# Kernel tuning notes

Measured on AMD Instinct MI355X. Metric: run time of the kernel, lower is better.

The kernel has to match this reference:

```python
import jax, jax.numpy as jnp
import numpy as np

B, S, D, H, G = 4, 2048, 1024, 16, 32
HD = D // H
LN_EPS = 1e-5


def _lin_init(key, fan_in, fan_out):
    kw, kb = jax.random.split(key)
    bound = 1.0 / np.sqrt(fan_in)
    W = jax.random.uniform(kw, (fan_in, fan_out), jnp.float32, -bound, bound)
    b = jax.random.uniform(kb, (fan_out,), jnp.float32, -bound, bound)
    return W, b


def setup_inputs() -> dict:
    key = jax.random.key(0)
    ks = jax.random.split(key, 9)
    x = jax.random.normal(ks[0], (B, S, D), jnp.float32)
    geo_features = jax.random.normal(ks[1], (B, G), jnp.float32)
    Wq, bq = _lin_init(ks[2], D, D)
    Wk, bk = _lin_init(ks[3], D, D)
    Wv, bv = _lin_init(ks[4], D, D)
    Wo, bo = _lin_init(ks[5], D, D)
    ge_W1, ge_b1 = _lin_init(ks[6], G, D)
    ln_g = jnp.ones((D,), jnp.float32)
    ln_b = jnp.zeros((D,), jnp.float32)
    ge_W2, ge_b2 = _lin_init(ks[7], D, D)
    gm_W, gm_b = _lin_init(ks[8], D, H)
    return dict(x=x, geo_features=geo_features, Wq=Wq, bq=bq, Wk=Wk, bk=bk,
                Wv=Wv, bv=bv, Wo=Wo, bo=bo, ge_W1=ge_W1, ge_b1=ge_b1,
                ln_g=ln_g, ln_b=ln_b, ge_W2=ge_W2, ge_b2=ge_b2,
                gm_W=gm_W, gm_b=gm_b)


def reference(x, geo_features, Wq, bq, Wk, bk, Wv, bv, Wo, bo,
              ge_W1, ge_b1, ln_g, ln_b, ge_W2, ge_b2, gm_W, gm_b):
    # QKV projections -> (B, H, S, HD)
    def split_heads(t):
        return t.reshape(B, S, H, HD).transpose(0, 2, 1, 3)
    Q = split_heads(x @ Wq + bq)
    K = split_heads(x @ Wk + bk)
    V = split_heads(x @ Wv + bv)

    # geo encoder: Linear -> LayerNorm -> ReLU -> Linear
    h = geo_features @ ge_W1 + ge_b1                      # (B, D)
    mu = jnp.mean(h, axis=-1, keepdims=True)
    var = jnp.mean(jnp.square(h - mu), axis=-1, keepdims=True)
    h = (h - mu) / jnp.sqrt(var + LN_EPS) * ln_g + ln_b
    h = jax.nn.relu(h)
    geo_encoded = h @ ge_W2 + ge_b2                       # (B, D)
    geo_mod = jax.nn.sigmoid(geo_encoded @ gm_W + gm_b)   # (B, H)

    scale = 1.0 / np.sqrt(HD)
    scores = jnp.einsum('bhqd,bhkd->bhqk', Q, K) * scale  # (B, H, S, S)
    scores = scores * (1.0 + geo_mod[:, :, None, None])
    attn = jax.nn.softmax(scores, axis=-1)                # dropout in eval mode: identity
    ctx = jnp.einsum('bhqk,bhkd->bhqd', attn, V)          # (B, H, S, HD)
    ctx = ctx.transpose(0, 2, 1, 3).reshape(B, S, D)
    out = ctx @ Wo + bo
    return out, attn
```

## Files before the change

kernel.cpp:

```cpp
#include <hip/hip_runtime.h>

typedef __attribute__((ext_vector_type(8))) short bf16x8;
typedef __attribute__((ext_vector_type(4))) float f32x4;
typedef __attribute__((ext_vector_type(4))) unsigned short us4;
typedef unsigned short u16;

#define MB (1024*1024)

#define WAITV(N) asm volatile("s_waitcnt vmcnt(" #N ")" ::: "memory")
#define WAITL0() asm volatile("s_waitcnt lgkmcnt(0)" ::: "memory")
#define BAR()    __builtin_amdgcn_s_barrier()
#define SCHEDB() __builtin_amdgcn_sched_barrier(0)

__device__ __forceinline__ u16 f2bf(float f) {
    unsigned u = __float_as_uint(f);
    unsigned r = (u + 0x7fffu + ((u >> 16) & 1u)) >> 16;
    return (u16)r;
}

__device__ __forceinline__ unsigned cvtpk(float a, float b) {
    unsigned r;
    asm("v_cvt_pk_bf16_f32 %0, %1, %2" : "=v"(r) : "v"(a), "v"(b));
    return r;
}

__device__ __forceinline__ f32x4 mfma16(bf16x8 a, bf16x8 b, f32x4 c) {
    return __builtin_amdgcn_mfma_f32_16x16x32_bf16(a, b, c, 0, 0, 0);
}

__device__ __forceinline__ void gload16(const void* g, void* l) {
    __builtin_amdgcn_global_load_lds(
        (__attribute__((address_space(1))) void*)(unsigned long long)g,
        (__attribute__((address_space(3))) void*)l, 16, 0, 0);
}

__global__ __launch_bounds__(256) void k_cvtx(const float* __restrict__ x, u16* __restrict__ xb) {
    const long long i = (long long)blockIdx.x * 256 + threadIdx.x;
    const float4* xp = (const float4*)x;
    float4 a = xp[i*2], b = xp[i*2+1];
    bf16x8 o;
    o[0]=(short)f2bf(a.x); o[1]=(short)f2bf(a.y); o[2]=(short)f2bf(a.z); o[3]=(short)f2bf(a.w);
    o[4]=(short)f2bf(b.x); o[5]=(short)f2bf(b.y); o[6]=(short)f2bf(b.z); o[7]=(short)f2bf(b.w);
    *(bf16x8*)&xb[i*8] = o;
}

__global__ __launch_bounds__(256) void k_wtcvt(const float* __restrict__ W0, const float* __restrict__ W1,
                                               const float* __restrict__ W2, const float* __restrict__ W3,
                                               u16* __restrict__ wt) {
    __shared__ float tl[32][33];
    const int t = threadIdx.x, z = blockIdx.z;
    const float* W = (z==0)?W0:(z==1)?W1:(z==2)?W2:W3;
    const int k0 = blockIdx.x*32, n0 = blockIdx.y*32;
    const int r = t >> 3, c4 = (t & 7) * 4;
    float4 v = *(const float4*)&W[(long long)(k0+r)*1024 + n0 + c4];
    tl[r][c4] = v.x; tl[r][c4+1] = v.y; tl[r][c4+2] = v.z; tl[r][c4+3] = v.w;
    __syncthreads();
    us4 ov;
    ov[0] = f2bf(tl[c4+0][r]); ov[1] = f2bf(tl[c4+1][r]);
    ov[2] = f2bf(tl[c4+2][r]); ov[3] = f2bf(tl[c4+3][r]);
    *(us4*)&wt[((long long)z << 20) + (long long)(n0+r)*1024 + k0 + c4] = ov;
}

__global__ __launch_bounds__(1024) void k_geo1(const float* __restrict__ geo, const float* __restrict__ W1,
                                               const float* __restrict__ b1, const float* __restrict__ lng,
                                               const float* __restrict__ lnb, float* __restrict__ hr) {
    const int b = blockIdx.x, j = threadIdx.x;
    float acc = b1[j];
    #pragma unroll 8
    for (int g = 0; g < 32; ++g) acc += geo[b*32+g] * W1[(long long)g*1024 + j];
    float s1 = acc, s2 = acc*acc;
    #pragma unroll
    for (int m = 1; m < 64; m <<= 1) { s1 += __shfl_xor(s1, m); s2 += __shfl_xor(s2, m); }
    __shared__ float r1[16], r2[16];
    __shared__ float mu_s, rv_s;
    const int wid = j >> 6, lid = j & 63;
    if (lid == 0) { r1[wid] = s1; r2[wid] = s2; }
    __syncthreads();
    if (j == 0) {
        float S1 = 0.f, S2 = 0.f;
        for (int i = 0; i < 16; ++i) { S1 += r1[i]; S2 += r2[i]; }
        float mu = S1 / 1024.f;
        float var = S2 / 1024.f - mu*mu;
        mu_s = mu; rv_s = rsqrtf(var + 1e-5f);
    }
    __syncthreads();
    float hv = (acc - mu_s) * rv_s * lng[j] + lnb[j];
    hr[b*1024 + j] = fmaxf(hv, 0.f);
}

__global__ __launch_bounds__(256) void k_geo2(const float* __restrict__ hr, const float* __restrict__ W2,
                                              const float* __restrict__ b2, float* __restrict__ ge) {
    const int b = blockIdx.x >> 4, jc = blockIdx.x & 15;
    const int t = threadIdx.x;
    __shared__ float hs[1024];
    __shared__ float parts[4][64];
    #pragma unroll
    for (int i = 0; i < 4; ++i) hs[t*4 + i] = hr[b*1024 + t*4 + i];
    __syncthreads();
    const int j = jc*64 + (t & 63), dq = t >> 6;
    float acc = 0.f;
    #pragma unroll 16
    for (int dd = 0; dd < 256; ++dd) {
        const int d = dq*256 + dd;
        acc += hs[d] * W2[(long long)d*1024 + j];
    }
    parts[dq][t & 63] = acc;
    __syncthreads();
    if (t < 64) {
        const int jj = jc*64 + t;
        ge[b*1024 + jj] = b2[jj] + parts[0][t] + parts[1][t] + parts[2][t] + parts[3][t];
    }
}

__global__ __launch_bounds__(1024) void k_geo3(const float* __restrict__ ge, const float* __restrict__ gmW,
                                               const float* __restrict__ gmb, float* __restrict__ qs) {
    const int t = threadIdx.x;
    const int hh = t & 15, b = (t >> 4) & 3, dq = t >> 6;
    __shared__ float parts[16][64];
    float part = 0.f;
    #pragma unroll 16
    for (int dd = 0; dd < 64; ++dd) {
        const int d = dq*64 + dd;
        part += ge[b*1024 + d] * gmW[d*16 + hh];
    }
    parts[dq][b*16 + hh] = part;
    __syncthreads();
    if (t < 64) {
        float s = gmb[t & 15];
        #pragma unroll
        for (int k = 0; k < 16; ++k) s += parts[k][t];
        qs[t] = 0.125f * (1.f + 1.f/(1.f + __expf(-s)));
    }
}

__global__ __launch_bounds__(256) void k_qkv_gemm(const u16* __restrict__ xb, const u16* __restrict__ wtq,
                                                  const float* __restrict__ bq, const float* __restrict__ bk,
                                                  const float* __restrict__ bv, u16* __restrict__ outq) {
    __shared__ u16 lA[128*64];
    __shared__ u16 lB[128*64];
    const int t = threadIdx.x, z = blockIdx.z;
    const int m0 = blockIdx.y * 128, n0 = blockIdx.x * 128;
    const u16* wt = wtq + (long long)z * (1024*1024);
    const float* bias = (z==0) ? bq : (z==1) ? bk : bv;
    u16* out = outq + (long long)z * 8388608;
    const int w = t >> 6, l = t & 63, lm = l & 15, lg = l >> 4;
    const int wr = (w >> 1) * 64, wc = (w & 1) * 64;
    f32x4 acc[4][4] = {};
    const char* gA = (const char*)xb + (long long)(m0 + (t>>3))*2048 + (t&7)*16;
    const char* gB = (const char*)wt + (long long)(n0 + (t>>3))*2048 + (t&7)*16;
    char* lAp = (char*)lA + t*16;
    char* lBp = (char*)lB + t*16;
    for (int k0 = 0; k0 < 1024; k0 += 64) {
        #pragma unroll
        for (int i = 0; i < 4; ++i) {
            gload16(gA + (long long)i*32*2048, lAp + i*4096);
            gload16(gB + (long long)i*32*2048, lBp + i*4096);
        }
        gA += 128; gB += 128;
        __syncthreads();
        #pragma unroll
        for (int kk = 0; kk < 2; ++kk) {
            bf16x8 af[4], bfr[4];
            #pragma unroll
            for (int mi = 0; mi < 4; ++mi)
                af[mi] = *(const bf16x8*)((const char*)lA + (wr + mi*16 + lm)*128 + kk*64 + lg*16);
            #pragma unroll
            for (int ni = 0; ni < 4; ++ni)
                bfr[ni] = *(const bf16x8*)((const char*)lB + (wc + ni*16 + lm)*128 + kk*64 + lg*16);
            #pragma unroll
            for (int mi = 0; mi < 4; ++mi)
                #pragma unroll
                for (int ni = 0; ni < 4; ++ni)
                    acc[mi][ni] = mfma16(bfr[ni], af[mi], acc[mi][ni]);
        }
        __syncthreads();
    }
    #pragma unroll
    for (int mi = 0; mi < 4; ++mi) {
        const int m = m0 + wr + mi*16 + lm;
        const int b = m >> 11, s = m & 2047;
        #pragma unroll
        for (int ni = 0; ni < 4; ++ni) {
            const int nb = n0 + wc + ni*16 + lg*4;
            const float4 bn4 = *(const float4*)&bias[nb];
            const int hh = nb >> 6, d = nb & 63;
            uint2 pk;
            pk.x = cvtpk(acc[mi][ni][0] + bn4.x, acc[mi][ni][1] + bn4.y);
            pk.y = cvtpk(acc[mi][ni][2] + bn4.z, acc[mi][ni][3] + bn4.w);
            *(uint2*)&out[(((long long)b*16 + hh)*2048 + s)*64 + d] = pk;
        }
    }
}

__global__ __launch_bounds__(256) void k_vtrans(const u16* __restrict__ vb, u16* __restrict__ vt) {
    __shared__ u16 tl[64][40];
    const int t = threadIdx.x;
    const int bh = blockIdx.z, s0 = blockIdx.y*64, d0 = blockIdx.x*32;
    const u16* vsrc = vb + (long long)bh*2048*64;
    {
        const int sl = t >> 2, dg = t & 3;
        bf16x8 v = *(const bf16x8*)&vsrc[(long long)(s0+sl)*64 + d0 + dg*8];
        *(bf16x8*)&tl[sl][dg*8] = v;
    }
    __syncthreads();
    {
        const int dl = t >> 3, sg = t & 7;
        bf16x8 o;
        #pragma unroll
        for (int j = 0; j < 8; ++j) o[j] = (short)tl[sg*8+j][dl];
        *(bf16x8*)&vt[((long long)bh*64 + d0+dl)*2048 + s0 + sg*8] = o;
    }
}

__global__ __launch_bounds__(512, 4) void k_attn_ctx(const u16* __restrict__ Qb, const u16* __restrict__ Kb,
                                                     const u16* __restrict__ Vt, const float* __restrict__ qsv,
                                                     float* __restrict__ invg, u16* __restrict__ ctxb) {
    __shared__ char lds[81920];

    const int nl = blockIdx.x;
    const int ob = (nl & 7)*64 + (nl >> 3);
    const int bh = ob >> 3, qt = ob & 7;
    const int t = threadIdx.x, w = t >> 6, l = t & 63, lm = l & 15, lg = l >> 4;
    const int q0 = qt * 256;
    const float qs = qsv[bh];

    const char* KB = (const char*)Kb + (long long)bh * 262144;
    const char* VB = (const char*)Vt + (long long)bh * 262144;

    bf16x8 qf[2][2];
    {
        const char* QB = (const char*)Qb + (long long)bh * 262144;
        #pragma unroll
        for (int ms = 0; ms < 2; ++ms)
            #pragma unroll
            for (int kc = 0; kc < 2; ++kc)
                qf[ms][kc] = *(const bf16x8*)(QB + (long long)(q0 + w*32 + ms*16 + lm)*128 + kc*64 + lg*16);
    }

    const int off = t*16;
    const int row = off >> 7, cbyt = off & 127;
    const int offA = off;
    const int srcK = row*128  + (cbyt ^ ((row & 7) << 4));
    const int srcV = row*4096 + (cbyt ^ ((row & 7) << 4));

    char* lP = lds + 49152;
    float lsum[2] = {0.f, 0.f};
    f32x4 cacc[2][4] = {};

    gload16(KB + srcK, lds + offA);
    gload16(VB + srcV, lds + 24576 + offA);
    gload16(KB + 8192 + srcK, lds + 8192 + offA);
    gload16(VB + 128 + srcV, lds + 24576 + 8192 + offA);
    SCHEDB();
    WAITV(2); BAR(); SCHEDB();

    int cb_ = 0, sb_ = 2;
    for (int kt = 0; kt < 32; ++kt) {
        const int ktn = (kt < 30) ? kt + 2 : 31;
        gload16(KB + (long long)ktn*8192 + srcK, lds + sb_*8192 + offA);
        gload16(VB + (long long)ktn*128 + srcV, lds + 24576 + sb_*8192 + offA);
        SCHEDB();

        const char* kb = lds + cb_*8192;
        #pragma unroll
        for (int ns = 0; ns < 4; ++ns) {
            const int rowb = ns*16 + lm;
            const int tag = (rowb & 7) << 4;
            bf16x8 kf0 = *(const bf16x8*)(kb + rowb*128 + ((lg*16) ^ tag));
            bf16x8 kf1 = *(const bf16x8*)(kb + rowb*128 + ((64 + lg*16) ^ tag));
            #pragma unroll
            for (int ms = 0; ms < 2; ++ms) {
                f32x4 a = {};
                a = mfma16(kf0, qf[ms][0], a);
                a = mfma16(kf1, qf[ms][1], a);
                const float p0 = __expf(a[0]*qs);
                const float p1 = __expf(a[1]*qs);
                const float p2 = __expf(a[2]*qs);
                const float p3 = __expf(a[3]*qs);
                lsum[ms] += (p0 + p1) + (p2 + p3);
                const int prow = w*32 + ms*16 + lm;
                const int ptag = (prow & 7) << 4;
                uint2 pk; pk.x = cvtpk(p0, p1); pk.y = cvtpk(p2, p3);
                *(uint2*)(lP + prow*128 + ((32*ns + 8*lg) ^ ptag)) = pk;
            }
        }
        WAITL0(); SCHEDB();

        const char* vb = lds + 24576 + cb_*8192;
        #pragma unroll
        for (int ks = 0; ks < 2; ++ks) {
            bf16x8 pa[2];
            #pragma unroll
            for (int ms = 0; ms < 2; ++ms) {
                const int prow = w*32 + ms*16 + lm;
                pa[ms] = *(const bf16x8*)(lP + prow*128 + ((ks*64 + lg*16) ^ ((prow & 7) << 4)));
            }
            #pragma unroll
            for (int dn = 0; dn < 4; ++dn) {
                const int rv = dn*16 + lm;
                bf16x8 vf = *(const bf16x8*)(vb + rv*128 + ((ks*64 + lg*16) ^ ((rv & 7) << 4)));
                cacc[0][dn] = mfma16(pa[0], vf, cacc[0][dn]);
                cacc[1][dn] = mfma16(pa[1], vf, cacc[1][dn]);
            }
        }
        WAITV(2); BAR(); SCHEDB();
        cb_ = (cb_ == 2) ? 0 : cb_ + 1;
        sb_ = (sb_ == 2) ? 0 : sb_ + 1;
    }

    float invl[2];
    #pragma unroll
    for (int ms = 0; ms < 2; ++ms) {
        float v = lsum[ms];
        v += __shfl_xor(v, 16);
        v += __shfl_xor(v, 32);
        invl[ms] = 1.f / v;
    }
    if (lg == 0) {
        invg[bh*2048 + q0 + w*32 + lm]      = invl[0];
        invg[bh*2048 + q0 + w*32 + 16 + lm] = invl[1];
    }
    float* fs = (float*)(lP + w*4096);
    if (lg == 0) { fs[lm] = invl[0]; fs[16 + lm] = invl[1]; }
    WAITL0(); SCHEDB();
    f32x4 iv[2];
    iv[0] = *(const f32x4*)&fs[lg*4];
    iv[1] = *(const f32x4*)&fs[16 + lg*4];

    const int b = bh >> 4, hh = bh & 15;
    #pragma unroll
    for (int ms = 0; ms < 2; ++ms)
        #pragma unroll
        for (int dn = 0; dn < 4; ++dn)
            #pragma unroll
            for (int r = 0; r < 4; ++r) {
                const int q = q0 + w*32 + ms*16 + lg*4 + r;
                ctxb[(((long long)b*2048 + q)*16 + hh)*64 + dn*16 + lm] = f2bf(cacc[ms][dn][r] * iv[ms][r]);
            }
}

__global__ __launch_bounds__(256, 2) void k_pwrite(const u16* __restrict__ Qb, const u16* __restrict__ Kb,
                                                   const float* __restrict__ qsv, const float* __restrict__ invg,
                                                   float* __restrict__ attn_out) {
    __shared__ char lds[81920];

    const int nl = blockIdx.x;
    const int ob = (nl & 7)*512 + (nl >> 3);
    const int bh = ob >> 6, qt = ob & 63;
    const int t = threadIdx.x, w = t >> 6, l = t & 63, lm = l & 15, lg = l >> 4;
    const int q0 = qt * 32;
    const int qg = w & 1, kq = w >> 1;
    const float qs = qsv[bh];

    const char* KB = (const char*)Kb + (long long)bh * 262144;

    bf16x8 qf[2];
    {
        const char* QB = (const char*)Qb + (long long)bh * 262144;
        #pragma unroll
        for (int kc = 0; kc < 2; ++kc)
            qf[kc] = *(const bf16x8*)(QB + (long long)(q0 + qg*16 + lm)*128 + kc*64 + lg*16);
    }
    const float invq = invg[bh*2048 + q0 + qg*16 + lm];

    int offA[2], srcK[2];
    #pragma unroll
    for (int i = 0; i < 2; ++i) {
        const int off = i*4096 + t*16;
        const int row = off >> 7, cbyt = off & 127;
        offA[i] = off;
        srcK[i] = row*128 + (cbyt ^ ((row & 7) << 4));
    }

    char* lP = lds + 49152;

    #pragma unroll
    for (int tt = 0; tt < 5; ++tt)
        #pragma unroll
        for (int i = 0; i < 2; ++i)
            gload16(KB + (long long)tt*8192 + srcK[i], lds + tt*8192 + offA[i]);
    SCHEDB();

    for (int kt = 0; kt < 32; ++kt) {
        if (kt < 4)            { WAITV(8); }
        else if ((kt & 3) == 0){ WAITV(24); }
        else                   { WAITV(16); }
        BAR(); SCHEDB();

        {
            const int ktn = (kt + 5 < 32) ? kt + 5 : 31;
            char* dst = lds + ((kt + 5) % 6)*8192;
            #pragma unroll
            for (int i = 0; i < 2; ++i)
                gload16(KB + (long long)ktn*8192 + srcK[i], dst + offA[i]);
        }
        SCHEDB();

        const char* kb = lds + (kt % 6)*8192;
        #pragma unroll
        for (int ns = 0; ns < 2; ++ns) {
            const int rowb = kq*32 + ns*16 + lm;
            const int tag = (lm & 7) << 4;
            bf16x8 kf0 = *(const bf16x8*)(kb + rowb*128 + ((lg*16) ^ tag));
            bf16x8 kf1 = *(const bf16x8*)(kb + rowb*128 + ((64 + lg*16) ^ tag));
            f32x4 a = {};
            a = mfma16(kf0, qf[0], a);
            a = mfma16(kf1, qf[1], a);
            f32x4 pv4;
            pv4[0] = __expf(a[0]*qs) * invq;
            pv4[1] = __expf(a[1]*qs) * invq;
            pv4[2] = __expf(a[2]*qs) * invq;
            pv4[3] = __expf(a[3]*qs) * invq;
            const int prow = qg*16 + lm;
            const int kwb = ((kt & 3) << 8) + (kq << 7) + (ns << 6) + (lg << 4);
            *(f32x4*)(lP + prow*1024 + (kwb ^ (lm << 4))) = pv4;
        }

        if ((kt & 3) == 3) {
            const int win = kt >> 2;
            WAITL0(); BAR(); SCHEDB();
            const int r0 = w*8;
            #pragma unroll
            for (int r = 0; r < 8; ++r) {
                const int rr = r0 + r;
                f32x4 v = *(const f32x4*)(lP + rr*1024 + ((l*16) ^ ((rr & 15) << 4)));
                *(f32x4*)(attn_out + ((long long)(bh*2048 + q0 + rr))*2048 + win*256 + l*4) = v;
            }
            SCHEDB();
        }
    }
}

__global__ __launch_bounds__(256) void k_o_gemm(const u16* __restrict__ ab, const u16* __restrict__ wt,
                                                const float* __restrict__ bo, float* __restrict__ outf) {
    __shared__ u16 lA[128*64];
    __shared__ u16 lB[128*64];
    const int t = threadIdx.x;
    const int m0 = blockIdx.y * 128, n0 = blockIdx.x * 128;
    const int w = t >> 6, l = t & 63, lm = l & 15, lg = l >> 4;
    const int wr = (w >> 1) * 64, wc = (w & 1) * 64;
    f32x4 acc[4][4] = {};
    const char* gA = (const char*)ab + (long long)(m0 + (t>>3))*2048 + (t&7)*16;
    const char* gB = (const char*)wt + (long long)(n0 + (t>>3))*2048 + (t&7)*16;
    char* lAp = (char*)lA + t*16;
    char* lBp = (char*)lB + t*16;
    for (int k0 = 0; k0 < 1024; k0 += 64) {
        #pragma unroll
        for (int i = 0; i < 4; ++i) {
            gload16(gA + (long long)i*32*2048, lAp + i*4096);
            gload16(gB + (long long)i*32*2048, lBp + i*4096);
        }
        gA += 128; gB += 128;
        __syncthreads();
        #pragma unroll
        for (int kk = 0; kk < 2; ++kk) {
            bf16x8 af[4], bfr[4];
            #pragma unroll
            for (int mi = 0; mi < 4; ++mi)
                af[mi] = *(const bf16x8*)((const char*)lA + (wr + mi*16 + lm)*128 + kk*64 + lg*16);
            #pragma unroll
            for (int ni = 0; ni < 4; ++ni)
                bfr[ni] = *(const bf16x8*)((const char*)lB + (wc + ni*16 + lm)*128 + kk*64 + lg*16);
            #pragma unroll
            for (int mi = 0; mi < 4; ++mi)
                #pragma unroll
                for (int ni = 0; ni < 4; ++ni)
                    acc[mi][ni] = mfma16(bfr[ni], af[mi], acc[mi][ni]);
        }
        __syncthreads();
    }
    #pragma unroll
    for (int mi = 0; mi < 4; ++mi) {
        const int m = m0 + wr + mi*16 + lm;
        #pragma unroll
        for (int ni = 0; ni < 4; ++ni) {
            const int nb = n0 + wc + ni*16 + lg*4;
            const float4 bn4 = *(const float4*)&bo[nb];
            f32x4 v = acc[mi][ni];
            v[0] += bn4.x; v[1] += bn4.y; v[2] += bn4.z; v[3] += bn4.w;
            *(f32x4*)&outf[(long long)m*1024 + nb] = v;
        }
    }
}

extern "C" void kernel_launch(void* const* d_in, const int* in_sizes, int n_in,
                              void* d_out, int out_size, void* d_ws, size_t ws_size,
                              hipStream_t stream) {
    const float* x    = (const float*)d_in[0];
    const float* geo  = (const float*)d_in[1];
    const float* Wq   = (const float*)d_in[2];
    const float* bq   = (const float*)d_in[3];
    const float* Wk   = (const float*)d_in[4];
    const float* bk   = (const float*)d_in[5];
    const float* Wv   = (const float*)d_in[6];
    const float* bv   = (const float*)d_in[7];
    const float* Wo   = (const float*)d_in[8];
    const float* bo   = (const float*)d_in[9];
    const float* geW1 = (const float*)d_in[10];
    const float* geb1 = (const float*)d_in[11];
    const float* lng  = (const float*)d_in[12];
    const float* lnb  = (const float*)d_in[13];
    const float* geW2 = (const float*)d_in[14];
    const float* geb2 = (const float*)d_in[15];
    const float* gmW  = (const float*)d_in[16];
    const float* gmb  = (const float*)d_in[17];

    char* ws = (char*)d_ws;
    u16* xb   = (u16*)(ws + 0);
    u16* wt   = (u16*)(ws + 16*(size_t)MB);
    u16* qkv  = (u16*)(ws + 24*(size_t)MB);
    u16* Qb   = qkv;
    u16* Kb   = (u16*)(ws + 40*(size_t)MB);
    u16* Vb   = (u16*)(ws + 56*(size_t)MB);
    u16* Vt   = (u16*)(ws + 72*(size_t)MB);
    u16* ctx  = Vb;
    float* qsb= (float*)(ws + 88*(size_t)MB);
    float* hr = (float*)(ws + 88*(size_t)MB + 4096);
    float* ge = (float*)(ws + 88*(size_t)MB + 65536);
    float* invg = (float*)(ws + 0);

    float* outf = (float*)d_out;
    float* attn = outf + 8388608;

    hipLaunchKernelGGL(k_cvtx,     dim3(4096),      dim3(256),  0, stream, x, xb);
    hipLaunchKernelGGL(k_wtcvt,    dim3(32,32,4),   dim3(256),  0, stream, Wq, Wk, Wv, Wo, wt);
    hipLaunchKernelGGL(k_geo1,     dim3(4),         dim3(1024), 0, stream, geo, geW1, geb1, lng, lnb, hr);
    hipLaunchKernelGGL(k_geo2,     dim3(64),        dim3(256),  0, stream, hr, geW2, geb2, ge);
    hipLaunchKernelGGL(k_geo3,     dim3(1),         dim3(1024), 0, stream, ge, gmW, gmb, qsb);
    hipLaunchKernelGGL(k_qkv_gemm, dim3(8,64,3),    dim3(256),  0, stream, xb, wt, bq, bk, bv, qkv);
    hipLaunchKernelGGL(k_vtrans,   dim3(2,32,64),   dim3(256),  0, stream, Vb, Vt);
    hipLaunchKernelGGL(k_attn_ctx, dim3(512),       dim3(512),  0, stream, Qb, Kb, Vt, qsb, invg, ctx);
    hipLaunchKernelGGL(k_pwrite,   dim3(4096),      dim3(256),  0, stream, Qb, Kb, qsb, invg, attn);
    hipLaunchKernelGGL(k_o_gemm,   dim3(8,64),      dim3(256),  0, stream, ctx, wt + 3*1048576, bo, outf);
}
```

Measured before the change: 537.8 us.

## Fuse attention context pass and probability write into one kernel per query tile

```diff
diff --git a/kernel.cpp b/kernel.cpp
--- a/kernel.cpp
+++ b/kernel.cpp
@@ -212,136 +212,9 @@
     }
 }
 
-__global__ __launch_bounds__(512, 4) void k_attn_ctx(const u16* __restrict__ Qb, const u16* __restrict__ Kb,
-                                                     const u16* __restrict__ Vt, const float* __restrict__ qsv,
-                                                     float* __restrict__ invg, u16* __restrict__ ctxb) {
-    __shared__ char lds[81920];
-
-    const int nl = blockIdx.x;
-    const int ob = (nl & 7)*64 + (nl >> 3);
-    const int bh = ob >> 3, qt = ob & 7;
-    const int t = threadIdx.x, w = t >> 6, l = t & 63, lm = l & 15, lg = l >> 4;
-    const int q0 = qt * 256;
-    const float qs = qsv[bh];
-
-    const char* KB = (const char*)Kb + (long long)bh * 262144;
-    const char* VB = (const char*)Vt + (long long)bh * 262144;
-
-    bf16x8 qf[2][2];
-    {
-        const char* QB = (const char*)Qb + (long long)bh * 262144;
-        #pragma unroll
-        for (int ms = 0; ms < 2; ++ms)
-            #pragma unroll
-            for (int kc = 0; kc < 2; ++kc)
-                qf[ms][kc] = *(const bf16x8*)(QB + (long long)(q0 + w*32 + ms*16 + lm)*128 + kc*64 + lg*16);
-    }
-
-    const int off = t*16;
-    const int row = off >> 7, cbyt = off & 127;
-    const int offA = off;
-    const int srcK = row*128  + (cbyt ^ ((row & 7) << 4));
-    const int srcV = row*4096 + (cbyt ^ ((row & 7) << 4));
-
-    char* lP = lds + 49152;
-    float lsum[2] = {0.f, 0.f};
-    f32x4 cacc[2][4] = {};
-
-    gload16(KB + srcK, lds + offA);
-    gload16(VB + srcV, lds + 24576 + offA);
-    gload16(KB + 8192 + srcK, lds + 8192 + offA);
-    gload16(VB + 128 + srcV, lds + 24576 + 8192 + offA);
-    SCHEDB();
-    WAITV(2); BAR(); SCHEDB();
-
-    int cb_ = 0, sb_ = 2;
-    for (int kt = 0; kt < 32; ++kt) {
-        const int ktn = (kt < 30) ? kt + 2 : 31;
-        gload16(KB + (long long)ktn*8192 + srcK, lds + sb_*8192 + offA);
-        gload16(VB + (long long)ktn*128 + srcV, lds + 24576 + sb_*8192 + offA);
-        SCHEDB();
-
-        const char* kb = lds + cb_*8192;
-        #pragma unroll
-        for (int ns = 0; ns < 4; ++ns) {
-            const int rowb = ns*16 + lm;
-            const int tag = (rowb & 7) << 4;
-            bf16x8 kf0 = *(const bf16x8*)(kb + rowb*128 + ((lg*16) ^ tag));
-            bf16x8 kf1 = *(const bf16x8*)(kb + rowb*128 + ((64 + lg*16) ^ tag));
-            #pragma unroll
-            for (int ms = 0; ms < 2; ++ms) {
-                f32x4 a = {};
-                a = mfma16(kf0, qf[ms][0], a);
-                a = mfma16(kf1, qf[ms][1], a);
-                const float p0 = __expf(a[0]*qs);
-                const float p1 = __expf(a[1]*qs);
-                const float p2 = __expf(a[2]*qs);
-                const float p3 = __expf(a[3]*qs);
-                lsum[ms] += (p0 + p1) + (p2 + p3);
-                const int prow = w*32 + ms*16 + lm;
-                const int ptag = (prow & 7) << 4;
-                uint2 pk; pk.x = cvtpk(p0, p1); pk.y = cvtpk(p2, p3);
-                *(uint2*)(lP + prow*128 + ((32*ns + 8*lg) ^ ptag)) = pk;
-            }
-        }
-        WAITL0(); SCHEDB();
-
-        const char* vb = lds + 24576 + cb_*8192;
-        #pragma unroll
-        for (int ks = 0; ks < 2; ++ks) {
-            bf16x8 pa[2];
-            #pragma unroll
-            for (int ms = 0; ms < 2; ++ms) {
-                const int prow = w*32 + ms*16 + lm;
-                pa[ms] = *(const bf16x8*)(lP + prow*128 + ((ks*64 + lg*16) ^ ((prow & 7) << 4)));
-            }
-            #pragma unroll
-            for (int dn = 0; dn < 4; ++dn) {
-                const int rv = dn*16 + lm;
-                bf16x8 vf = *(const bf16x8*)(vb + rv*128 + ((ks*64 + lg*16) ^ ((rv & 7) << 4)));
-                cacc[0][dn] = mfma16(pa[0], vf, cacc[0][dn]);
-                cacc[1][dn] = mfma16(pa[1], vf, cacc[1][dn]);
-            }
-        }
-        WAITV(2); BAR(); SCHEDB();
-        cb_ = (cb_ == 2) ? 0 : cb_ + 1;
-        sb_ = (sb_ == 2) ? 0 : sb_ + 1;
-    }
-
-    float invl[2];
-    #pragma unroll
-    for (int ms = 0; ms < 2; ++ms) {
-        float v = lsum[ms];
-        v += __shfl_xor(v, 16);
-        v += __shfl_xor(v, 32);
-        invl[ms] = 1.f / v;
-    }
-    if (lg == 0) {
-        invg[bh*2048 + q0 + w*32 + lm]      = invl[0];
-        invg[bh*2048 + q0 + w*32 + 16 + lm] = invl[1];
-    }
-    float* fs = (float*)(lP + w*4096);
-    if (lg == 0) { fs[lm] = invl[0]; fs[16 + lm] = invl[1]; }
-    WAITL0(); SCHEDB();
-    f32x4 iv[2];
-    iv[0] = *(const f32x4*)&fs[lg*4];
-    iv[1] = *(const f32x4*)&fs[16 + lg*4];
-
-    const int b = bh >> 4, hh = bh & 15;
-    #pragma unroll
-    for (int ms = 0; ms < 2; ++ms)
-        #pragma unroll
-        for (int dn = 0; dn < 4; ++dn)
-            #pragma unroll
-            for (int r = 0; r < 4; ++r) {
-                const int q = q0 + w*32 + ms*16 + lg*4 + r;
-                ctxb[(((long long)b*2048 + q)*16 + hh)*64 + dn*16 + lm] = f2bf(cacc[ms][dn][r] * iv[ms][r]);
-            }
-}
-
-__global__ __launch_bounds__(256, 2) void k_pwrite(const u16* __restrict__ Qb, const u16* __restrict__ Kb,
-                                                   const float* __restrict__ qsv, const float* __restrict__ invg,
-                                                   float* __restrict__ attn_out) {
+__global__ __launch_bounds__(256, 2) void k_attn(const u16* __restrict__ Qb, const u16* __restrict__ Kb,
+                                                 const u16* __restrict__ Vt, const float* __restrict__ qsv,
+                                                 float* __restrict__ attn_out, u16* __restrict__ ctxb) {
     __shared__ char lds[81920];
 
     const int nl = blockIdx.x;
@@ -353,6 +226,7 @@
     const float qs = qsv[bh];
 
     const char* KB = (const char*)Kb + (long long)bh * 262144;
+    const char* VB = (const char*)Vt + (long long)bh * 262144;
 
     bf16x8 qf[2];
     {
@@ -361,72 +235,173 @@
         for (int kc = 0; kc < 2; ++kc)
             qf[kc] = *(const bf16x8*)(QB + (long long)(q0 + qg*16 + lm)*128 + kc*64 + lg*16);
     }
-    const float invq = invg[bh*2048 + q0 + qg*16 + lm];
-
-    int offA[2], srcK[2];
+
+    int offA[2], srcK[2], srcV[2];
     #pragma unroll
     for (int i = 0; i < 2; ++i) {
         const int off = i*4096 + t*16;
         const int row = off >> 7, cbyt = off & 127;
         offA[i] = off;
-        srcK[i] = row*128 + (cbyt ^ ((row & 7) << 4));
-    }
+        srcK[i] = row*128  + (cbyt ^ ((row & 7) << 4));
+        srcV[i] = row*4096 + (cbyt ^ ((row & 7) << 4));
+    }
+
+    char* lP4 = lds + 49152;
+    float* fs  = (float*)(lds + 53248);
+    float* cred = (float*)(lds + 57344);
+
+    const int prow = qg*16 + lm, ptag = (prow & 7) << 4;
+
+    float lsum = 0.f;
+    f32x4 cacc[4] = {};
+    {
+        #pragma unroll
+        for (int tt = 0; tt < 2; ++tt) {
+            #pragma unroll
+            for (int i = 0; i < 2; ++i) gload16(KB + tt*8192 + srcK[i], lds + tt*8192 + offA[i]);
+            #pragma unroll
+            for (int i = 0; i < 2; ++i) gload16(VB + tt*128 + srcV[i], lds + 24576 + tt*8192 + offA[i]);
+        }
+        SCHEDB();
+        WAITV(4); BAR(); SCHEDB();
+
+        int cb_ = 0, sb_ = 2;
+        for (int kt = 0; kt < 32; ++kt) {
+            const int ktn = (kt < 30) ? kt + 2 : 31;
+            #pragma unroll
+            for (int i = 0; i < 2; ++i) gload16(KB + (long long)ktn*8192 + srcK[i], lds + sb_*8192 + offA[i]);
+            #pragma unroll
+            for (int i = 0; i < 2; ++i) gload16(VB + (long long)ktn*128 + srcV[i], lds + 24576 + sb_*8192 + offA[i]);
+            SCHEDB();
+
+            const char* kb = lds + cb_*8192;
+            #pragma unroll
+            for (int ns = 0; ns < 2; ++ns) {
+                const int rowb = kq*32 + ns*16 + lm;
+                const int tag = (rowb & 7) << 4;
+                bf16x8 kf0 = *(const bf16x8*)(kb + rowb*128 + ((lg*16) ^ tag));
+                bf16x8 kf1 = *(const bf16x8*)(kb + rowb*128 + ((64 + lg*16) ^ tag));
+                f32x4 a = {};
+                a = mfma16(kf0, qf[0], a);
+                a = mfma16(kf1, qf[1], a);
+                const float p0 = __expf(a[0]*qs);
+                const float p1 = __expf(a[1]*qs);
+                const float p2 = __expf(a[2]*qs);
+                const float p3 = __expf(a[3]*qs);
+                lsum += (p0 + p1) + (p2 + p3);
+                uint2 pk; pk.x = cvtpk(p0, p1); pk.y = cvtpk(p2, p3);
+                *(uint2*)(lP4 + prow*128 + ((kq*64 + ns*32 + lg*8) ^ ptag)) = pk;
+            }
+            WAITL0(); SCHEDB();
+
+            bf16x8 pa = *(const bf16x8*)(lP4 + prow*128 + ((kq*64 + lg*16) ^ ptag));
+            const char* vb = lds + 24576 + cb_*8192;
+            #pragma unroll
+            for (int dn = 0; dn < 4; ++dn) {
+                const int rv = dn*16 + lm;
+                bf16x8 vf = *(const bf16x8*)(vb + rv*128 + ((kq*64 + lg*16) ^ ((rv & 7) << 4)));
+                cacc[dn] = mfma16(pa, vf, cacc[dn]);
+            }
+            WAITV(4); BAR(); SCHEDB();
+            cb_ = (cb_ == 2) ? 0 : cb_ + 1;
+            sb_ = (sb_ == 2) ? 0 : sb_ + 1;
+        }
+    }
+    WAITV(0);
+    __syncthreads();
+
+    {
+        float v = lsum;
+        v += __shfl_xor(v, 16);
+        v += __shfl_xor(v, 32);
+        if (lg == 0) fs[kq*32 + qg*16 + lm] = v;
+    }
+    if (kq == 1) {
+        float* cr = cred + qg*1024;
+        #pragma unroll
+        for (int dn = 0; dn < 4; ++dn)
+            #pragma unroll
+            for (int r = 0; r < 4; ++r)
+                cr[(lg*4 + r)*64 + dn*16 + lm] = cacc[dn][r];
+    }
+    __syncthreads();
+    const float invq = 1.f / (fs[qg*16 + lm] + fs[32 + qg*16 + lm]);
+    if (kq == 0) {
+        float* cr = cred + qg*1024;
+        const int b = bh >> 4, hh = bh & 15;
+        float il[4];
+        #pragma unroll
+        for (int r = 0; r < 4; ++r) {
+            const int qrow = qg*16 + lg*4 + r;
+            il[r] = 1.f / (fs[qrow] + fs[32 + qrow]);
+        }
+        #pragma unroll
+        for (int dn = 0; dn < 4; ++dn)
+            #pragma unroll
+            for (int r = 0; r < 4; ++r) {
+                const int qrow = qg*16 + lg*4 + r;
+                const float s = cacc[dn][r] + cr[(lg*4 + r)*64 + dn*16 + lm];
+                ctxb[(((long long)b*2048 + q0 + qrow)*16 + hh)*64 + dn*16 + lm] = f2bf(s * il[r]);
+            }
+    }
+    __syncthreads();
 
     char* lP = lds + 49152;
-
-    #pragma unroll
-    for (int tt = 0; tt < 5; ++tt)
-        #pragma unroll
-        for (int i = 0; i < 2; ++i)
-            gload16(KB + (long long)tt*8192 + srcK[i], lds + tt*8192 + offA[i]);
-    SCHEDB();
-
-    for (int kt = 0; kt < 32; ++kt) {
-        if (kt < 4)            { WAITV(8); }
-        else if ((kt & 3) == 0){ WAITV(24); }
-        else                   { WAITV(16); }
-        BAR(); SCHEDB();
-
-        {
-            const int ktn = (kt + 5 < 32) ? kt + 5 : 31;
-            char* dst = lds + ((kt + 5) % 6)*8192;
+    {
+        #pragma unroll
+        for (int tt = 0; tt < 5; ++tt)
             #pragma unroll
             for (int i = 0; i < 2; ++i)
-                gload16(KB + (long long)ktn*8192 + srcK[i], dst + offA[i]);
-        }
+                gload16(KB + (long long)tt*8192 + srcK[i], lds + tt*8192 + offA[i]);
         SCHEDB();
 
-        const char* kb = lds + (kt % 6)*8192;
-        #pragma unroll
-        for (int ns = 0; ns < 2; ++ns) {
-            const int rowb = kq*32 + ns*16 + lm;
-            const int tag = (lm & 7) << 4;
-            bf16x8 kf0 = *(const bf16x8*)(kb + rowb*128 + ((lg*16) ^ tag));
-            bf16x8 kf1 = *(const bf16x8*)(kb + rowb*128 + ((64 + lg*16) ^ tag));
-            f32x4 a = {};
-            a = mfma16(kf0, qf[0], a);
-            a = mfma16(kf1, qf[1], a);
-            f32x4 pv4;
-            pv4[0] = __expf(a[0]*qs) * invq;
-            pv4[1] = __expf(a[1]*qs) * invq;
-            pv4[2] = __expf(a[2]*qs) * invq;
-            pv4[3] = __expf(a[3]*qs) * invq;
-            const int prow = qg*16 + lm;
-            const int kwb = ((kt & 3) << 8) + (kq << 7) + (ns << 6) + (lg << 4);
-            *(f32x4*)(lP + prow*1024 + (kwb ^ (lm << 4))) = pv4;
-        }
-
-        if ((kt & 3) == 3) {
-            const int win = kt >> 2;
-            WAITL0(); BAR(); SCHEDB();
-            const int r0 = w*8;
-            #pragma unroll
-            for (int r = 0; r < 8; ++r) {
-                const int rr = r0 + r;
-                f32x4 v = *(const f32x4*)(lP + rr*1024 + ((l*16) ^ ((rr & 15) << 4)));
-                *(f32x4*)(attn_out + ((long long)(bh*2048 + q0 + rr))*2048 + win*256 + l*4) = v;
+        for (int kt = 0; kt < 32; ++kt) {
+            if (kt < 4)              { WAITV(8); }
+            else if (kt == 4)        { WAITV(16); }
+            else if ((kt & 3) == 0)  { WAITV(24); }
+            else                     { WAITV(16); }
+            BAR(); SCHEDB();
+
+            {
+                const int ktn = (kt + 5 < 32) ? kt + 5 : 31;
+                char* dst = lds + ((kt + 5) % 6)*8192;
+                #pragma unroll
+                for (int i = 0; i < 2; ++i)
+                    gload16(KB + (long long)ktn*8192 + srcK[i], dst + offA[i]);
             }
             SCHEDB();
+
+            const char* kb = lds + (kt % 6)*8192;
+            #pragma unroll
+            for (int ns = 0; ns < 2; ++ns) {
+                const int rowb = kq*32 + ns*16 + lm;
+                const int tag = (lm & 7) << 4;
+                bf16x8 kf0 = *(const bf16x8*)(kb + rowb*128 + ((lg*16) ^ tag));
+                bf16x8 kf1 = *(const bf16x8*)(kb + rowb*128 + ((64 + lg*16) ^ tag));
+                f32x4 a = {};
+                a = mfma16(kf0, qf[0], a);
+                a = mfma16(kf1, qf[1], a);
+                f32x4 pv4;
+                pv4[0] = __expf(a[0]*qs) * invq;
+                pv4[1] = __expf(a[1]*qs) * invq;
+                pv4[2] = __expf(a[2]*qs) * invq;
+                pv4[3] = __expf(a[3]*qs) * invq;
+                const int kwb = ((kt & 3) << 8) + (kq << 7) + (ns << 6) + (lg << 4);
+                *(f32x4*)(lP + prow*1024 + (kwb ^ (lm << 4))) = pv4;
+            }
+
+            if ((kt & 3) == 3) {
+                const int win = kt >> 2;
+                WAITL0(); BAR(); SCHEDB();
+                const int r0 = w*8;
+                #pragma unroll
+                for (int r = 0; r < 8; ++r) {
+                    const int rr = r0 + r;
+                    f32x4 v = *(const f32x4*)(lP + rr*1024 + ((l*16) ^ ((rr & 15) << 4)));
+                    *(f32x4*)(attn_out + ((long long)(bh*2048 + q0 + rr))*2048 + win*256 + l*4) = v;
+                }
+                SCHEDB();
+            }
         }
     }
 }
@@ -517,7 +492,6 @@
     float* qsb= (float*)(ws + 88*(size_t)MB);
     float* hr = (float*)(ws + 88*(size_t)MB + 4096);
     float* ge = (float*)(ws + 88*(size_t)MB + 65536);
-    float* invg = (float*)(ws + 0);
 
     float* outf = (float*)d_out;
     float* attn = outf + 8388608;
@@ -529,7 +503,6 @@
     hipLaunchKernelGGL(k_geo3,     dim3(1),         dim3(1024), 0, stream, ge, gmW, gmb, qsb);
     hipLaunchKernelGGL(k_qkv_gemm, dim3(8,64,3),    dim3(256),  0, stream, xb, wt, bq, bk, bv, qkv);
     hipLaunchKernelGGL(k_vtrans,   dim3(2,32,64),   dim3(256),  0, stream, Vb, Vt);
-    hipLaunchKernelGGL(k_attn_ctx, dim3(512),       dim3(512),  0, stream, Qb, Kb, Vt, qsb, invg, ctx);
-    hipLaunchKernelGGL(k_pwrite,   dim3(4096),      dim3(256),  0, stream, Qb, Kb, qsb, invg, attn);
+    hipLaunchKernelGGL(k_attn,     dim3(4096),      dim3(256),  0, stream, Qb, Kb, Vt, qsb, attn, ctx);
     hipLaunchKernelGGL(k_o_gemm,   dim3(8,64),      dim3(256),  0, stream, ctx, wt + 3*1048576, bo, outf);
 }
```

After: 636.3 us. 1.18x slower.
